# Kernel optimization log

Measured on AMD Instinct MI355X. Metric: run time of the kernel, lower is better.

The kernel has to match this reference:

```python
import jax, jax.numpy as jnp
import numpy as np

EPS = 1e-5

def _layernorm(x, g, b):
    mu = jnp.mean(x, axis=-1, keepdims=True)
    var = jnp.mean(jnp.square(x - mu), axis=-1, keepdims=True)
    return (x - mu) * jax.lax.rsqrt(var + EPS) * g + b

def setup_inputs() -> dict:
    key = jax.random.key(0)
    ks = jax.random.split(key, 5)
    F_, H, D = 1024, 16, 64
    B, N = 4, 2048
    s = lambda k, shp, fan: jax.random.normal(k, shp, jnp.float32) * (fan ** -0.5)
    return {
        "x": jax.random.normal(ks[0], (B, N, F_), jnp.float32),
        "Wq": s(ks[1], (H * D, F_), F_),
        "Wkv": s(ks[2], (2 * H * D, F_), F_),
        "Wo": s(ks[3], (F_, H * D), H * D),
        "ln_g": jnp.ones((F_,), jnp.float32),
        "ln_b": jnp.zeros((F_,), jnp.float32),
        "lnc_g": jnp.ones((F_,), jnp.float32),
        "lnc_b": jnp.zeros((F_,), jnp.float32),
    }

def reference(x, Wq, Wkv, Wo, ln_g, ln_b, lnc_g, lnc_b):
    H, D = 16, 64
    scale = D ** -0.5
    skip = x
    xn = _layernorm(x, ln_g, ln_b)          # query path norm
    cn = _layernorm(x, lnc_g, lnc_b)        # context (self) norm
    B, N, _ = x.shape
    q = jnp.einsum('bnf,ef->bne', xn, Wq)   # [B,N,H*D]
    kv = jnp.einsum('bnf,ef->bne', cn, Wkv) # [B,N,2*H*D]
    k, v = jnp.split(kv, 2, axis=-1)
    tohd = lambda t: t.reshape(B, N, H, D).transpose(0, 2, 1, 3)  # b h n d
    q, k, v = tohd(q), tohd(k), tohd(v)
    sim = jnp.einsum('bhnd,bhmd->bhnm', q, k) * scale
    attn = jax.nn.softmax(sim, axis=-1)
    out = jnp.einsum('bhnm,bhmd->bhnd', attn, v)
    out = out.transpose(0, 2, 1, 3).reshape(B, N, H * D)
    out = jnp.einsum('bne,fe->bnf', out, Wo)
    return skip + out
```

## Files before the change

### kernel.cpp

```cpp
#include <hip/hip_runtime.h>
#include <hip/hip_bf16.h>
#include <stdint.h>

typedef __bf16 bf16;
typedef __bf16 bf16x8 __attribute__((ext_vector_type(8)));
typedef __bf16 bf16x4 __attribute__((ext_vector_type(4)));
typedef float f32x4 __attribute__((ext_vector_type(4)));
typedef unsigned u32x2 __attribute__((ext_vector_type(2)));

#define F_DIM 1024
#define NSEQ  2048
#define NB    4
#define NH    16
#define HD    64
#define MROWS (NB * NSEQ)
#define LOG2E 1.44269504088896340736f

__device__ __forceinline__ void gload_lds16(const void* g, void* l) {
    __builtin_amdgcn_global_load_lds(
        (__attribute__((address_space(1))) void*)g,
        (__attribute__((address_space(3))) void*)l,
        16, 0, 0);
}

__device__ __forceinline__ unsigned lds_addr(const void* p) {
    return (unsigned)(size_t)(__attribute__((address_space(3))) const void*)p;
}

__device__ __forceinline__ float exp2_fast(float x) {
    float r;
    asm("v_exp_f32 %0, %1" : "=v"(r) : "v"(x));
    return r;
}

__device__ __forceinline__ unsigned cvtpk_bf16(float lo, float hi) {
    unsigned r;
    asm("v_cvt_pk_bf16_f32 %0, %1, %2" : "=v"(r) : "v"(lo), "v"(hi));
    return r;
}

__global__ __launch_bounds__(256) void ln2_kernel(
    const float* __restrict__ x,
    const float* __restrict__ g1, const float* __restrict__ b1,
    const float* __restrict__ g2, const float* __restrict__ b2,
    bf16* __restrict__ xn, bf16* __restrict__ cn)
{
    const int row = blockIdx.x;
    const int t = threadIdx.x;
    float4 v = reinterpret_cast<const float4*>(x + (size_t)row * F_DIM)[t];
    float s  = v.x + v.y + v.z + v.w;
    float ss = v.x * v.x + v.y * v.y + v.z * v.z + v.w * v.w;
#pragma unroll
    for (int m = 1; m < 64; m <<= 1) {
        s  += __shfl_xor(s, m);
        ss += __shfl_xor(ss, m);
    }
    __shared__ float red[8];
    const int w = t >> 6;
    if ((t & 63) == 0) { red[w] = s; red[4 + w] = ss; }
    __syncthreads();
    s  = red[0] + red[1] + red[2] + red[3];
    ss = red[4] + red[5] + red[6] + red[7];
    const float mu  = s * (1.0f / F_DIM);
    const float var = fmaxf(ss * (1.0f / F_DIM) - mu * mu, 0.0f);
    const float rs  = rsqrtf(var + 1e-5f);

    float4 G1 = reinterpret_cast<const float4*>(g1)[t];
    float4 B1 = reinterpret_cast<const float4*>(b1)[t];
    float4 G2 = reinterpret_cast<const float4*>(g2)[t];
    float4 B2 = reinterpret_cast<const float4*>(b2)[t];
    const float h0 = (v.x - mu) * rs, h1 = (v.y - mu) * rs;
    const float h2 = (v.z - mu) * rs, h3 = (v.w - mu) * rs;
    bf16x4 o1 = { (bf16)(h0 * G1.x + B1.x), (bf16)(h1 * G1.y + B1.y),
                  (bf16)(h2 * G1.z + B1.z), (bf16)(h3 * G1.w + B1.w) };
    bf16x4 o2 = { (bf16)(h0 * G2.x + B2.x), (bf16)(h1 * G2.y + B2.y),
                  (bf16)(h2 * G2.z + B2.z), (bf16)(h3 * G2.w + B2.w) };
    *reinterpret_cast<bf16x4*>(xn + (size_t)row * F_DIM + t * 4) = o1;
    *reinterpret_cast<bf16x4*>(cn + (size_t)row * F_DIM + t * 4) = o2;
}

__global__ __launch_bounds__(256) void cvt3_kernel(
    const float* __restrict__ wq, const float* __restrict__ wkv,
    const float* __restrict__ wo, bf16* __restrict__ dst)
{
    const int i = blockIdx.x * 256 + threadIdx.x;
    const float* src;
    int si;
    if (i < 262144)       { src = wq;  si = i; }
    else if (i < 786432)  { src = wkv; si = i - 262144; }
    else                  { src = wo;  si = i - 786432; }
    float4 v = reinterpret_cast<const float4*>(src)[si];
    bf16x4 o = { (bf16)v.x, (bf16)v.y, (bf16)v.z, (bf16)v.w };
    reinterpret_cast<bf16x4*>(dst)[i] = o;
}

__global__ __launch_bounds__(256, 2) void qkv_gemm(
    const bf16* __restrict__ xn, const bf16* __restrict__ cn,
    const bf16* __restrict__ wq, const bf16* __restrict__ wkv,
    bf16* __restrict__ qb, bf16* __restrict__ kvb, float qscale)
{
    __shared__ bf16 As[128 * 32];
    __shared__ bf16 Bs[128 * 32];
    const int t = threadIdx.x;
    const int lane = t & 63;
    const int w = t >> 6;
    const int wr = w >> 1, wc = w & 1;

    int flat = blockIdx.x;
    flat = (flat & 7) * 192 + (flat >> 3);

    const bf16 *A, *B;
    bf16* C;
    int N, bm, bn;
    float osc;
    if (flat < 512) {
        A = xn; B = wq; C = qb; N = 1024; osc = qscale;
        bm = (flat >> 3) * 128; bn = (flat & 7) * 128;
    } else {
        const int f = flat - 512;
        A = cn; B = wkv; C = kvb; N = 2048; osc = 1.0f;
        bm = (f >> 4) * 128; bn = (f & 15) * 128;
    }

    const int r = lane & 15;
    const int kg = (lane >> 4) * 8;

    f32x4 acc[4][4];
#pragma unroll
    for (int i = 0; i < 4; i++)
#pragma unroll
        for (int j = 0; j < 4; j++) acc[i][j] = (f32x4){0.f, 0.f, 0.f, 0.f};

    const int c0 = t, c1 = 256 + t;
    const size_t aoff0 = (size_t)(bm + (c0 >> 2)) * F_DIM + (c0 & 3) * 8;
    const size_t aoff1 = (size_t)(bm + (c1 >> 2)) * F_DIM + (c1 & 3) * 8;
    const size_t boff0 = (size_t)(bn + (c0 >> 2)) * F_DIM + (c0 & 3) * 8;
    const size_t boff1 = (size_t)(bn + (c1 >> 2)) * F_DIM + (c1 & 3) * 8;
    bf16* lA0 = As + (size_t)(0 * 256 + w * 64) * 8;
    bf16* lA1 = As + (size_t)(1 * 256 + w * 64) * 8;
    bf16* lB0 = Bs + (size_t)(0 * 256 + w * 64) * 8;
    bf16* lB1 = Bs + (size_t)(1 * 256 + w * 64) * 8;

    for (int kt = 0; kt < F_DIM; kt += 32) {
        gload_lds16(A + aoff0 + kt, lA0);
        gload_lds16(A + aoff1 + kt, lA1);
        gload_lds16(B + boff0 + kt, lB0);
        gload_lds16(B + boff1 + kt, lB1);
        __syncthreads();
        bf16x8 af[4], bfr[4];
#pragma unroll
        for (int mi = 0; mi < 4; mi++)
            af[mi] = *(const bf16x8*)(As + (wr * 64 + mi * 16 + r) * 32 + kg);
#pragma unroll
        for (int ni = 0; ni < 4; ni++)
            bfr[ni] = *(const bf16x8*)(Bs + (wc * 64 + ni * 16 + r) * 32 + kg);
#pragma unroll
        for (int mi = 0; mi < 4; mi++)
#pragma unroll
            for (int ni = 0; ni < 4; ni++)
                acc[mi][ni] = __builtin_amdgcn_mfma_f32_16x16x32_bf16(
                    af[mi], bfr[ni], acc[mi][ni], 0, 0, 0);
        __syncthreads();
    }

    const int g = lane >> 4;
#pragma unroll
    for (int mi = 0; mi < 4; mi++) {
#pragma unroll
        for (int ni = 0; ni < 4; ni++) {
            const int col = bn + wc * 64 + ni * 16 + r;
#pragma unroll
            for (int j = 0; j < 4; j++) {
                const int row = bm + wr * 64 + mi * 16 + g * 4 + j;
                C[(size_t)row * N + col] = (bf16)(acc[mi][ni][j] * osc);
            }
        }
    }
}

__global__ __launch_bounds__(256, 2) void o_gemm(
    const bf16* __restrict__ A, const bf16* __restrict__ B,
    float* __restrict__ Cf, const float* __restrict__ skip)
{
    __shared__ bf16 As[128 * 32];
    __shared__ bf16 Bs[128 * 32];
    const int t = threadIdx.x;
    const int lane = t & 63;
    const int w = t >> 6;
    const int wr = w >> 1, wc = w & 1;

    int flat = blockIdx.x;
    flat = (flat & 7) * 64 + (flat >> 3);
    const int bm = (flat >> 3) * 128;
    const int bn = (flat & 7) * 128;

    const int r = lane & 15;
    const int kg = (lane >> 4) * 8;

    f32x4 acc[4][4];
#pragma unroll
    for (int i = 0; i < 4; i++)
#pragma unroll
        for (int j = 0; j < 4; j++) acc[i][j] = (f32x4){0.f, 0.f, 0.f, 0.f};

    const int c0 = t, c1 = 256 + t;
    const size_t aoff0 = (size_t)(bm + (c0 >> 2)) * F_DIM + (c0 & 3) * 8;
    const size_t aoff1 = (size_t)(bm + (c1 >> 2)) * F_DIM + (c1 & 3) * 8;
    const size_t boff0 = (size_t)(bn + (c0 >> 2)) * F_DIM + (c0 & 3) * 8;
    const size_t boff1 = (size_t)(bn + (c1 >> 2)) * F_DIM + (c1 & 3) * 8;
    bf16* lA0 = As + (size_t)(0 * 256 + w * 64) * 8;
    bf16* lA1 = As + (size_t)(1 * 256 + w * 64) * 8;
    bf16* lB0 = Bs + (size_t)(0 * 256 + w * 64) * 8;
    bf16* lB1 = Bs + (size_t)(1 * 256 + w * 64) * 8;

    for (int kt = 0; kt < F_DIM; kt += 32) {
        gload_lds16(A + aoff0 + kt, lA0);
        gload_lds16(A + aoff1 + kt, lA1);
        gload_lds16(B + boff0 + kt, lB0);
        gload_lds16(B + boff1 + kt, lB1);
        __syncthreads();
        bf16x8 af[4], bfr[4];
#pragma unroll
        for (int mi = 0; mi < 4; mi++)
            af[mi] = *(const bf16x8*)(As + (wr * 64 + mi * 16 + r) * 32 + kg);
#pragma unroll
        for (int ni = 0; ni < 4; ni++)
            bfr[ni] = *(const bf16x8*)(Bs + (wc * 64 + ni * 16 + r) * 32 + kg);
#pragma unroll
        for (int mi = 0; mi < 4; mi++)
#pragma unroll
            for (int ni = 0; ni < 4; ni++)
                acc[mi][ni] = __builtin_amdgcn_mfma_f32_16x16x32_bf16(
                    af[mi], bfr[ni], acc[mi][ni], 0, 0, 0);
        __syncthreads();
    }

    const int g = lane >> 4;
#pragma unroll
    for (int mi = 0; mi < 4; mi++) {
#pragma unroll
        for (int ni = 0; ni < 4; ni++) {
            const int col = bn + wc * 64 + ni * 16 + r;
#pragma unroll
            for (int j = 0; j < 4; j++) {
                const int row = bm + wr * 64 + mi * 16 + g * 4 + j;
                Cf[(size_t)row * F_DIM + col] =
                    acc[mi][ni][j] + skip[(size_t)row * F_DIM + col];
            }
        }
    }
}

__global__ __launch_bounds__(512)
__attribute__((amdgpu_waves_per_eu(4, 5)))
void attn_kernel(
    const bf16* __restrict__ q, const bf16* __restrict__ kvp,
    bf16* __restrict__ o)
{
    __shared__ __align__(16) bf16 Ks[128 * 64];
    __shared__ __align__(16) bf16 Vs[128 * 64];
    __shared__ __align__(16) bf16 Ps[8][16 * 72];

    const int bid = blockIdx.x;
    const int idx = (bid & 7) * 128 + (bid >> 3);
    const int bh = idx >> 4;
    const int qt = idx & 15;
    const int b = bh >> 4, h = bh & 15;

    const int t = threadIdx.x, lane = t & 63, w = t >> 6;
    const int r = lane & 15, g = lane >> 4;

    const size_t rowq = (size_t)b * NSEQ;

    size_t ksrc[2], vsrc[2];
#pragma unroll
    for (int c = 0; c < 2; c++) {
        const int p = c * 512 + t;
        const int krow = p >> 3;
        const int kcol = (p & 7) ^ (krow & 7);
        ksrc[c] = (size_t)(rowq + krow) * (2 * F_DIM) + h * HD + kcol * 8;
        const int kvb = p >> 5, dblk = (p >> 3) & 3;
        const int kvl = (p & 7) >> 1, d8 = p & 1;
        vsrc[c] = (size_t)(rowq + kvb * 4 + kvl) * (2 * F_DIM) + F_DIM + h * HD
                  + dblk * 16 + d8 * 8;
    }

    const int q0 = qt * 128 + w * 16;
    bf16x8 qf[2];
#pragma unroll
    for (int kk = 0; kk < 2; kk++)
        qf[kk] = *(const bf16x8*)(q + (rowq + q0 + r) * F_DIM + h * HD + kk * 32 + g * 8);

    f32x4 oacc[4];
#pragma unroll
    for (int i = 0; i < 4; i++) oacc[i] = (f32x4){0.f, 0.f, 0.f, 0.f};
    float m_r = -1e30f, l_r = 0.f;

    const unsigned va    = lds_addr(Vs) + (unsigned)(g * 1024 + r * 8);
    const unsigned pbase = lds_addr(&Ps[w][0]) + (unsigned)((r * 72 + g * 8) * 2);

    for (int kv0 = 0; kv0 < NSEQ; kv0 += 128) {
        asm volatile("s_barrier" ::: "memory");
        const size_t koff = (size_t)kv0 * (2 * F_DIM);
#pragma unroll
        for (int c = 0; c < 2; c++) {
            gload_lds16(kvp + ksrc[c] + koff, Ks + (size_t)(c * 512 + (t & ~63)) * 8);
            gload_lds16(kvp + vsrc[c] + koff, Vs + (size_t)(c * 512 + (t & ~63)) * 8);
        }
        asm volatile("s_waitcnt vmcnt(0)\n\ts_barrier" ::: "memory");

        f32x4 s4[8];
#pragma unroll
        for (int nt = 0; nt < 8; nt++) s4[nt] = (f32x4){0.f, 0.f, 0.f, 0.f};
        __builtin_amdgcn_s_setprio(1);
#pragma unroll
        for (int kk = 0; kk < 2; kk++) {
#pragma unroll
            for (int nt = 0; nt < 8; nt++) {
                const unsigned lb = (unsigned)((nt * 16 + r) * 128 + kk * 64 + g * 16)
                                    ^ (unsigned)((r & 7) << 4);
                bf16x8 kf = *(const bf16x8*)((const char*)Ks + lb);
                s4[nt] = __builtin_amdgcn_mfma_f32_16x16x32_bf16(kf, qf[kk], s4[nt], 0, 0, 0);
            }
        }
        __builtin_amdgcn_s_setprio(0);

        float mx = s4[0][0];
#pragma unroll
        for (int nt = 0; nt < 8; nt++)
#pragma unroll
            for (int j = 0; j < 4; j++) mx = fmaxf(mx, s4[nt][j]);
        mx = fmaxf(mx, __shfl_xor(mx, 16));
        mx = fmaxf(mx, __shfl_xor(mx, 32));
        if (!__all(mx <= m_r + 8.0f)) {
            const float mnew = fmaxf(m_r, mx);
            const float alpha = exp2_fast(m_r - mnew);
            l_r *= alpha;
#pragma unroll
            for (int j = 0; j < 4; j++) {
                const float aj = __shfl(alpha, g * 4 + j);
#pragma unroll
                for (int ntd = 0; ntd < 4; ntd++) oacc[ntd][j] *= aj;
            }
            m_r = mnew;
        }
        u32x2 pa2[8];
        float ps = 0.f;
#pragma unroll
        for (int nt = 0; nt < 8; nt++) {
            const float e0 = exp2_fast(s4[nt][0] - m_r);
            const float e1 = exp2_fast(s4[nt][1] - m_r);
            const float e2 = exp2_fast(s4[nt][2] - m_r);
            const float e3 = exp2_fast(s4[nt][3] - m_r);
            ps += (e0 + e1) + (e2 + e3);
            pa2[nt] = (u32x2){ cvtpk_bf16(e0, e1), cvtpk_bf16(e2, e3) };
        }
        ps += __shfl_xor(ps, 16);
        ps += __shfl_xor(ps, 32);
        l_r += ps;

#pragma unroll
        for (int hh = 0; hh < 2; hh++) {
#pragma unroll
            for (int nt2 = 0; nt2 < 4; nt2++)
                *(u32x2*)&Ps[w][r * 72 + nt2 * 16 + g * 4] = pa2[hh * 4 + nt2];
            asm volatile("s_waitcnt lgkmcnt(0)" ::: "memory");

            bf16x8 pf[2];
            u32x2 vt[2][4][2];
#pragma unroll
            for (int kk2 = 0; kk2 < 2; kk2++) {
                const unsigned pa = pbase + (unsigned)(kk2 * 64);
                asm volatile("ds_read_b128 %0, %1" : "=v"(pf[kk2]) : "v"(pa));
                const int kkg = hh * 2 + kk2;
#pragma unroll
                for (int ntd = 0; ntd < 4; ntd++) {
                    const unsigned a = va + (unsigned)(kkg * 4096 + ntd * 128);
                    asm volatile("ds_read_b64_tr_b16 %0, %2\n\t"
                                 "ds_read_b64_tr_b16 %1, %2 offset:512"
                                 : "=&v"(vt[kk2][ntd][0]), "=&v"(vt[kk2][ntd][1])
                                 : "v"(a));
                }
            }
            asm volatile("s_waitcnt lgkmcnt(0)" ::: "memory");
            __builtin_amdgcn_sched_barrier(0);

            __builtin_amdgcn_s_setprio(1);
#pragma unroll
            for (int kk2 = 0; kk2 < 2; kk2++)
#pragma unroll
                for (int ntd = 0; ntd < 4; ntd++) {
                    union { u32x2 hl[2]; bf16x8 v; } u;
                    u.hl[0] = vt[kk2][ntd][0];
                    u.hl[1] = vt[kk2][ntd][1];
                    oacc[ntd] = __builtin_amdgcn_mfma_f32_16x16x32_bf16(pf[kk2], u.v, oacc[ntd], 0, 0, 0);
                }
            __builtin_amdgcn_s_setprio(0);
        }
    }

    float rl[4];
#pragma unroll
    for (int j = 0; j < 4; j++) {
        const float lj = __shfl(l_r, g * 4 + j);
        rl[j] = 1.0f / lj;
    }
#pragma unroll
    for (int ntd = 0; ntd < 4; ntd++)
#pragma unroll
        for (int j = 0; j < 4; j++) {
            const int row = q0 + g * 4 + j;
            o[(rowq + row) * F_DIM + h * HD + ntd * 16 + r] =
                (bf16)(oacc[ntd][j] * rl[j]);
        }
}

extern "C" void kernel_launch(void* const* d_in, const int* in_sizes, int n_in,
                              void* d_out, int out_size, void* d_ws, size_t ws_size,
                              hipStream_t stream)
{
    const float* x     = (const float*)d_in[0];
    const float* Wq    = (const float*)d_in[1];
    const float* Wkv   = (const float*)d_in[2];
    const float* Wo    = (const float*)d_in[3];
    const float* ln_g  = (const float*)d_in[4];
    const float* ln_b  = (const float*)d_in[5];
    const float* lnc_g = (const float*)d_in[6];
    const float* lnc_b = (const float*)d_in[7];
    float* out = (float*)d_out;

    bf16* xn   = (bf16*)d_ws;
    bf16* cn   = xn  + (size_t)MROWS * F_DIM;
    bf16* qb   = cn  + (size_t)MROWS * F_DIM;
    bf16* kvb  = qb  + (size_t)MROWS * F_DIM;
    bf16* wqb  = kvb + (size_t)MROWS * 2 * F_DIM;
    bf16* wkvb = wqb + (size_t)F_DIM * F_DIM;
    bf16* wob  = wkvb + (size_t)2 * F_DIM * F_DIM;
    bf16* ao   = xn;

    ln2_kernel<<<dim3(MROWS), dim3(256), 0, stream>>>(x, ln_g, ln_b, lnc_g, lnc_b, xn, cn);

    cvt3_kernel<<<dim3(4096), dim3(256), 0, stream>>>(Wq, Wkv, Wo, wqb);

    qkv_gemm<<<dim3(1536), dim3(256), 0, stream>>>(
        xn, cn, wqb, wkvb, qb, kvb, 0.125f * LOG2E);
    attn_kernel<<<dim3(NSEQ / 128 * NB * NH), dim3(512), 0, stream>>>(qb, kvb, ao);
    o_gemm<<<dim3(512), dim3(256), 0, stream>>>(ao, wob, out, x);
}
```

Measured before the change: 216.2 us.

## Process two query tiles per attention block to reuse loaded K/V tiles

Each attention workgroup now handles 256 query rows, with each wave owning two 16-row query slices, so every K/V tile loaded into LDS is used twice. The grid is halved and the block-to-(batch,head,qtile) mapping adjusted. This cuts global K/V traffic and barrier overhead per query, in exchange for more registers per thread (double accumulators and softmax state), a relaxed waves-per-EU hint, and fewer blocks to spread across CUs (512 vs 1024).

```diff
diff --git a/kernel.cpp b/kernel.cpp
--- a/kernel.cpp
+++ b/kernel.cpp
@@ -252,7 +252,7 @@
 }
 
 __global__ __launch_bounds__(512)
-__attribute__((amdgpu_waves_per_eu(4, 5)))
+__attribute__((amdgpu_waves_per_eu(2, 4)))
 void attn_kernel(
     const bf16* __restrict__ q, const bf16* __restrict__ kvp,
     bf16* __restrict__ o)
@@ -262,9 +262,9 @@
     __shared__ __align__(16) bf16 Ps[8][16 * 72];
 
     const int bid = blockIdx.x;
-    const int idx = (bid & 7) * 128 + (bid >> 3);
-    const int bh = idx >> 4;
-    const int qt = idx & 15;
+    const int idx = (bid & 7) * 64 + (bid >> 3);
+    const int bh = idx >> 3;
+    const int qt = idx & 7;
     const int b = bh >> 4, h = bh & 15;
 
     const int t = threadIdx.x, lane = t & 63, w = t >> 6;
@@ -285,16 +285,21 @@
                   + dblk * 16 + d8 * 8;
     }
 
-    const int q0 = qt * 128 + w * 16;
-    bf16x8 qf[2];
-#pragma unroll
-    for (int kk = 0; kk < 2; kk++)
-        qf[kk] = *(const bf16x8*)(q + (rowq + q0 + r) * F_DIM + h * HD + kk * 32 + g * 8);
-
-    f32x4 oacc[4];
-#pragma unroll
-    for (int i = 0; i < 4; i++) oacc[i] = (f32x4){0.f, 0.f, 0.f, 0.f};
-    float m_r = -1e30f, l_r = 0.f;
+    const int q0 = qt * 256 + w * 16;
+    bf16x8 qf[2][2];
+#pragma unroll
+    for (int qi = 0; qi < 2; qi++)
+#pragma unroll
+        for (int kk = 0; kk < 2; kk++)
+            qf[qi][kk] = *(const bf16x8*)(q + (rowq + q0 + qi * 128 + r) * F_DIM
+                                          + h * HD + kk * 32 + g * 8);
+
+    f32x4 oacc[2][4];
+#pragma unroll
+    for (int qi = 0; qi < 2; qi++)
+#pragma unroll
+        for (int i = 0; i < 4; i++) oacc[qi][i] = (f32x4){0.f, 0.f, 0.f, 0.f};
+    float m_r[2] = { -1e30f, -1e30f }, l_r[2] = { 0.f, 0.f };
 
     const unsigned va    = lds_addr(Vs) + (unsigned)(g * 1024 + r * 8);
     const unsigned pbase = lds_addr(&Ps[w][0]) + (unsigned)((r * 72 + g * 8) * 2);
@@ -309,110 +314,117 @@
         }
         asm volatile("s_waitcnt vmcnt(0)\n\ts_barrier" ::: "memory");
 
-        f32x4 s4[8];
-#pragma unroll
-        for (int nt = 0; nt < 8; nt++) s4[nt] = (f32x4){0.f, 0.f, 0.f, 0.f};
-        __builtin_amdgcn_s_setprio(1);
-#pragma unroll
-        for (int kk = 0; kk < 2; kk++) {
+#pragma unroll
+        for (int qi = 0; qi < 2; qi++) {
+            f32x4 s4[8];
+#pragma unroll
+            for (int nt = 0; nt < 8; nt++) s4[nt] = (f32x4){0.f, 0.f, 0.f, 0.f};
+            __builtin_amdgcn_s_setprio(1);
+#pragma unroll
+            for (int kk = 0; kk < 2; kk++) {
+#pragma unroll
+                for (int nt = 0; nt < 8; nt++) {
+                    const unsigned lb = (unsigned)((nt * 16 + r) * 128 + kk * 64 + g * 16)
+                                        ^ (unsigned)((r & 7) << 4);
+                    bf16x8 kf = *(const bf16x8*)((const char*)Ks + lb);
+                    s4[nt] = __builtin_amdgcn_mfma_f32_16x16x32_bf16(kf, qf[qi][kk], s4[nt], 0, 0, 0);
+                }
+            }
+            __builtin_amdgcn_s_setprio(0);
+
+            float mx = s4[0][0];
+#pragma unroll
+            for (int nt = 0; nt < 8; nt++)
+#pragma unroll
+                for (int j = 0; j < 4; j++) mx = fmaxf(mx, s4[nt][j]);
+            mx = fmaxf(mx, __shfl_xor(mx, 16));
+            mx = fmaxf(mx, __shfl_xor(mx, 32));
+            if (!__all(mx <= m_r[qi] + 8.0f)) {
+                const float mnew = fmaxf(m_r[qi], mx);
+                const float alpha = exp2_fast(m_r[qi] - mnew);
+                l_r[qi] *= alpha;
+#pragma unroll
+                for (int j = 0; j < 4; j++) {
+                    const float aj = __shfl(alpha, g * 4 + j);
+#pragma unroll
+                    for (int ntd = 0; ntd < 4; ntd++) oacc[qi][ntd][j] *= aj;
+                }
+                m_r[qi] = mnew;
+            }
+            u32x2 pa2[8];
+            float ps = 0.f;
 #pragma unroll
             for (int nt = 0; nt < 8; nt++) {
-                const unsigned lb = (unsigned)((nt * 16 + r) * 128 + kk * 64 + g * 16)
-                                    ^ (unsigned)((r & 7) << 4);
-                bf16x8 kf = *(const bf16x8*)((const char*)Ks + lb);
-                s4[nt] = __builtin_amdgcn_mfma_f32_16x16x32_bf16(kf, qf[kk], s4[nt], 0, 0, 0);
+                const float e0 = exp2_fast(s4[nt][0] - m_r[qi]);
+                const float e1 = exp2_fast(s4[nt][1] - m_r[qi]);
+                const float e2 = exp2_fast(s4[nt][2] - m_r[qi]);
+                const float e3 = exp2_fast(s4[nt][3] - m_r[qi]);
+                ps += (e0 + e1) + (e2 + e3);
+                pa2[nt] = (u32x2){ cvtpk_bf16(e0, e1), cvtpk_bf16(e2, e3) };
+            }
+            ps += __shfl_xor(ps, 16);
+            ps += __shfl_xor(ps, 32);
+            l_r[qi] += ps;
+
+#pragma unroll
+            for (int hh = 0; hh < 2; hh++) {
+#pragma unroll
+                for (int nt2 = 0; nt2 < 4; nt2++)
+                    *(u32x2*)&Ps[w][r * 72 + nt2 * 16 + g * 4] = pa2[hh * 4 + nt2];
+                asm volatile("s_waitcnt lgkmcnt(0)" ::: "memory");
+
+                bf16x8 pf[2];
+                u32x2 vt[2][4][2];
+#pragma unroll
+                for (int kk2 = 0; kk2 < 2; kk2++) {
+                    const unsigned pa = pbase + (unsigned)(kk2 * 64);
+                    asm volatile("ds_read_b128 %0, %1" : "=v"(pf[kk2]) : "v"(pa));
+                    const int kkg = hh * 2 + kk2;
+#pragma unroll
+                    for (int ntd = 0; ntd < 4; ntd++) {
+                        const unsigned a = va + (unsigned)(kkg * 4096 + ntd * 128);
+                        asm volatile("ds_read_b64_tr_b16 %0, %2\n\t"
+                                     "ds_read_b64_tr_b16 %1, %2 offset:512"
+                                     : "=&v"(vt[kk2][ntd][0]), "=&v"(vt[kk2][ntd][1])
+                                     : "v"(a));
+                    }
+                }
+                asm volatile("s_waitcnt lgkmcnt(0)" ::: "memory");
+                __builtin_amdgcn_sched_barrier(0);
+
+                __builtin_amdgcn_s_setprio(1);
+#pragma unroll
+                for (int kk2 = 0; kk2 < 2; kk2++)
+#pragma unroll
+                    for (int ntd = 0; ntd < 4; ntd++) {
+                        union { u32x2 hl[2]; bf16x8 v; } u;
+                        u.hl[0] = vt[kk2][ntd][0];
+                        u.hl[1] = vt[kk2][ntd][1];
+                        oacc[qi][ntd] = __builtin_amdgcn_mfma_f32_16x16x32_bf16(
+                            pf[kk2], u.v, oacc[qi][ntd], 0, 0, 0);
+                    }
+                __builtin_amdgcn_s_setprio(0);
             }
         }
-        __builtin_amdgcn_s_setprio(0);
-
-        float mx = s4[0][0];
-#pragma unroll
-        for (int nt = 0; nt < 8; nt++)
-#pragma unroll
-            for (int j = 0; j < 4; j++) mx = fmaxf(mx, s4[nt][j]);
-        mx = fmaxf(mx, __shfl_xor(mx, 16));
-        mx = fmaxf(mx, __shfl_xor(mx, 32));
-        if (!__all(mx <= m_r + 8.0f)) {
-            const float mnew = fmaxf(m_r, mx);
-            const float alpha = exp2_fast(m_r - mnew);
-            l_r *= alpha;
+    }
+
+#pragma unroll
+    for (int qi = 0; qi < 2; qi++) {
+        float rl[4];
+#pragma unroll
+        for (int j = 0; j < 4; j++) {
+            const float lj = __shfl(l_r[qi], g * 4 + j);
+            rl[j] = 1.0f / lj;
+        }
+#pragma unroll
+        for (int ntd = 0; ntd < 4; ntd++)
 #pragma unroll
             for (int j = 0; j < 4; j++) {
-                const float aj = __shfl(alpha, g * 4 + j);
-#pragma unroll
-                for (int ntd = 0; ntd < 4; ntd++) oacc[ntd][j] *= aj;
-            }
-            m_r = mnew;
-        }
-        u32x2 pa2[8];
-        float ps = 0.f;
-#pragma unroll
-        for (int nt = 0; nt < 8; nt++) {
-            const float e0 = exp2_fast(s4[nt][0] - m_r);
-            const float e1 = exp2_fast(s4[nt][1] - m_r);
-            const float e2 = exp2_fast(s4[nt][2] - m_r);
-            const float e3 = exp2_fast(s4[nt][3] - m_r);
-            ps += (e0 + e1) + (e2 + e3);
-            pa2[nt] = (u32x2){ cvtpk_bf16(e0, e1), cvtpk_bf16(e2, e3) };
-        }
-        ps += __shfl_xor(ps, 16);
-        ps += __shfl_xor(ps, 32);
-        l_r += ps;
-
-#pragma unroll
-        for (int hh = 0; hh < 2; hh++) {
-#pragma unroll
-            for (int nt2 = 0; nt2 < 4; nt2++)
-                *(u32x2*)&Ps[w][r * 72 + nt2 * 16 + g * 4] = pa2[hh * 4 + nt2];
-            asm volatile("s_waitcnt lgkmcnt(0)" ::: "memory");
-
-            bf16x8 pf[2];
-            u32x2 vt[2][4][2];
-#pragma unroll
-            for (int kk2 = 0; kk2 < 2; kk2++) {
-                const unsigned pa = pbase + (unsigned)(kk2 * 64);
-                asm volatile("ds_read_b128 %0, %1" : "=v"(pf[kk2]) : "v"(pa));
-                const int kkg = hh * 2 + kk2;
-#pragma unroll
-                for (int ntd = 0; ntd < 4; ntd++) {
-                    const unsigned a = va + (unsigned)(kkg * 4096 + ntd * 128);
-                    asm volatile("ds_read_b64_tr_b16 %0, %2\n\t"
-                                 "ds_read_b64_tr_b16 %1, %2 offset:512"
-                                 : "=&v"(vt[kk2][ntd][0]), "=&v"(vt[kk2][ntd][1])
-                                 : "v"(a));
-                }
-            }
-            asm volatile("s_waitcnt lgkmcnt(0)" ::: "memory");
-            __builtin_amdgcn_sched_barrier(0);
-
-            __builtin_amdgcn_s_setprio(1);
-#pragma unroll
-            for (int kk2 = 0; kk2 < 2; kk2++)
-#pragma unroll
-                for (int ntd = 0; ntd < 4; ntd++) {
-                    union { u32x2 hl[2]; bf16x8 v; } u;
-                    u.hl[0] = vt[kk2][ntd][0];
-                    u.hl[1] = vt[kk2][ntd][1];
-                    oacc[ntd] = __builtin_amdgcn_mfma_f32_16x16x32_bf16(pf[kk2], u.v, oacc[ntd], 0, 0, 0);
-                }
-            __builtin_amdgcn_s_setprio(0);
-        }
-    }
-
-    float rl[4];
-#pragma unroll
-    for (int j = 0; j < 4; j++) {
-        const float lj = __shfl(l_r, g * 4 + j);
-        rl[j] = 1.0f / lj;
-    }
-#pragma unroll
-    for (int ntd = 0; ntd < 4; ntd++)
-#pragma unroll
-        for (int j = 0; j < 4; j++) {
-            const int row = q0 + g * 4 + j;
-            o[(rowq + row) * F_DIM + h * HD + ntd * 16 + r] =
-                (bf16)(oacc[ntd][j] * rl[j]);
-        }
+                const int row = q0 + qi * 128 + g * 4 + j;
+                o[(rowq + row) * F_DIM + h * HD + ntd * 16 + r] =
+                    (bf16)(oacc[qi][ntd][j] * rl[j]);
+            }
+    }
 }
 
 extern "C" void kernel_launch(void* const* d_in, const int* in_sizes, int n_in,
@@ -444,6 +456,6 @@
 
     qkv_gemm<<<dim3(1536), dim3(256), 0, stream>>>(
         xn, cn, wqb, wkvb, qb, kvb, 0.125f * LOG2E);
-    attn_kernel<<<dim3(NSEQ / 128 * NB * NH), dim3(512), 0, stream>>>(qb, kvb, ao);
+    attn_kernel<<<dim3(NSEQ / 256 * NB * NH), dim3(512), 0, stream>>>(qb, kvb, ao);
     o_gemm<<<dim3(512), dim3(256), 0, stream>>>(ao, wob, out, x);
 }
```

Measured after the change: 233.1 us. 7.8% more time.
